# Optimization experiments

Measured on AMD Instinct MI355X. Metric: run time of the kernel, lower is better.

## Reference

```python
import jax, jax.numpy as jnp
import numpy as np

NEG_SLOPE = 0.2   # RGATConv default negative_slope
BN_EPS = 1e-5     # torch BatchNorm1d default eps


def _build_edges(n0, n1, batch):
    """Replicates generate_edges_union + PyG Batch offsetting. Returns [2, B*E] src/dst and [B*E] edge types."""
    n = n0 + n1
    def perm(k, off):  # itertools.permutations(range(k), 2) as (src, dst) columns
        a = np.repeat(np.arange(k), k); b = np.tile(np.arange(k), k)
        m = a != b
        return np.stack([a[m], b[m]]) + off
    intra = np.concatenate([perm(n0, 0), perm(n1, n0)], axis=1)                 # edge_type 0
    ca = np.repeat(np.arange(n0), n1); cb = np.tile(np.arange(n0, n), n0)
    cross = np.concatenate([np.stack([ca, cb]), np.stack([cb, ca])], axis=1)    # edge_type 1
    edges = np.concatenate([intra, cross], axis=1)
    etype = np.concatenate([np.zeros(intra.shape[1], np.int32), np.ones(cross.shape[1], np.int32)])
    offs = (np.arange(batch) * n)[:, None, None]
    edges_b = (edges[None, :, :] + offs).transpose(1, 0, 2).reshape(2, -1)      # per-graph node offsets
    etype_b = np.tile(etype, batch)
    return jnp.asarray(edges_b, jnp.int32), jnp.asarray(etype_b, jnp.int32)


def _segment_softmax(logits, seg, num_seg):
    m = jax.ops.segment_max(logits, seg, num_segments=num_seg)
    m = jnp.where(jnp.isfinite(m), m, 0.0)
    e = jnp.exp(logits - m[seg])
    s = jax.ops.segment_sum(e, seg, num_segments=num_seg)
    return e / (s[seg] + 1e-16)  # PyG softmax eps


def _rgat_layer(x, src, dst, etype, W, q, k, b, num_nodes):
    # PyG RGATConv: heads=1, dim=1, concat=False, additive-self-attention, across-relation softmax, aggr=add
    H = jnp.einsum('nf,rfe->rne', x, W)            # relation-specific transform: [2, BN, F]
    qs = jnp.einsum('rne,e->rn', H, q)             # q-score per node per relation
    ks = jnp.einsum('rne,e->rn', H, k)
    logit = jax.nn.leaky_relu(qs[etype, dst] + ks[etype, src], NEG_SLOPE)  # [E]
    alpha = _segment_softmax(logit, dst, num_nodes)
    msg = alpha[:, None] * H[etype, src]           # [E, F] per-edge messages
    out = jax.ops.segment_sum(msg, dst, num_segments=num_nodes)
    return out + b                                 # heads=1 -> mean over heads is identity; + bias


def setup_inputs() -> dict:
    key = jax.random.key(0)
    ks = jax.random.split(key, 6)
    B, F, N0, N1, L = 4, 256, 128, 128, 3
    s = 0.05
    return {
        'desc0': jax.random.normal(ks[0], (B, F, N0), jnp.float32),
        'desc1': jax.random.normal(ks[1], (B, F, N1), jnp.float32),
        'conv_w': jax.random.normal(ks[2], (L, 2, F, F), jnp.float32) * s,
        'conv_q': jax.random.normal(ks[3], (L, F), jnp.float32) * s,
        'conv_k': jax.random.normal(ks[4], (L, F), jnp.float32) * s,
        'conv_b': jnp.zeros((L, F), jnp.float32),
        'lin_w': jax.random.normal(ks[5], (L, F, 2 * F), jnp.float32) * s,
        'lin_b': jnp.zeros((L, F), jnp.float32),
        'bn_w': jnp.ones((L, F), jnp.float32),
        'bn_b': jnp.zeros((L, F), jnp.float32),
    }


def reference(desc0, desc1, conv_w, conv_q, conv_k, conv_b, lin_w, lin_b, bn_w, bn_b):
    b, f, n0 = desc0.shape
    n1 = desc1.shape[2]
    n = n0 + n1
    # [B, F, N] -> batched node features [B*N, F]
    x = jnp.concatenate([desc0, desc1], axis=2).transpose(0, 2, 1).reshape(b * n, f)
    edges, etype = _build_edges(n0, n1, b)
    src, dst = edges[0], edges[1]
    num_nodes = b * n
    for i in range(conv_w.shape[0]):
        msg1 = jax.nn.relu(_rgat_layer(x, src, dst, etype, conv_w[i], conv_q[i], conv_k[i], conv_b[i], num_nodes))
        msg2 = jnp.concatenate([x, msg1], axis=1) @ lin_w[i].T + lin_b[i]
        mu = msg2.mean(axis=0)
        var = msg2.var(axis=0)  # biased, as torch BatchNorm uses for normalization (training mode)
        msg3 = bn_w[i] * (msg2 - mu) / jnp.sqrt(var + BN_EPS) + bn_b[i]
        x = x + msg3            # edge_pool[i] == 1 -> no knn_graph rebuild
    x = x.reshape(b, n, f).transpose(0, 2, 1)
    return x[:, :, :n0], x[:, :, n0:]
```

## Files before the change

### kernel.cpp

```cpp
#include <hip/hip_runtime.h>
#include <math.h>


typedef __attribute__((ext_vector_type(8))) short short8;
typedef __attribute__((ext_vector_type(4))) float f32x4;
typedef unsigned short u16;
typedef unsigned int   u32;

__device__ __forceinline__ u16 f2bf(float f) {
    union { float f; u32 u; } v; v.f = f;
    u32 r = v.u + 0x7fffu + ((v.u >> 16) & 1u);
    return (u16)(r >> 16);
}
__device__ __forceinline__ short8 ld8(const u16* p) {
    return __builtin_bit_cast(short8, *(const int4*)p);
}

__global__ __launch_bounds__(256) void k_prep(
    const float* __restrict__ d0, const float* __restrict__ d1,
    const float* __restrict__ conv_w, const float* __restrict__ lin_w,
    float* __restrict__ x, u16* __restrict__ xb,
    u16* __restrict__ Wt, u16* __restrict__ lwb) {
    const int t = threadIdx.x;
    if (blockIdx.x < 256) {
        __shared__ float Ts[32 * 33];
        const int tt = blockIdx.x;
        const int b = tt >> 6, rem = tt & 63, ft = rem >> 3, nt = rem & 7;
        const float* src = (nt < 4) ? d0 : d1;
        const int nloc = (nt & 3) * 32;
        {
            int fr = t >> 3, c4 = t & 7;
            float4 v = *(const float4*)&src[b * 32768 + (ft * 32 + fr) * 128 + nloc + c4 * 4];
            Ts[fr * 33 + c4 * 4 + 0] = v.x;
            Ts[fr * 33 + c4 * 4 + 1] = v.y;
            Ts[fr * 33 + c4 * 4 + 2] = v.z;
            Ts[fr * 33 + c4 * 4 + 3] = v.w;
        }
        __syncthreads();
        {
            int nr = t >> 3, f4 = t & 7;
            float4 v;
            v.x = Ts[(f4 * 4 + 0) * 33 + nr];
            v.y = Ts[(f4 * 4 + 1) * 33 + nr];
            v.z = Ts[(f4 * 4 + 2) * 33 + nr];
            v.w = Ts[(f4 * 4 + 3) * 33 + nr];
            int node = b * 256 + nt * 32 + nr;
            int idx = node * 256 + ft * 32 + f4 * 4;
            *(float4*)&x[idx] = v;
            ushort4 hb = {f2bf(v.x), f2bf(v.y), f2bf(v.z), f2bf(v.w)};
            *(ushort4*)&xb[idx] = hb;
        }
    } else if (blockIdx.x < 640) {
        __shared__ float Ts[32 * 33];
        const int tt = blockIdx.x - 256;
        const int mat = tt >> 6, rem = tt & 63, et = rem >> 3, ft = rem & 7;
        {
            int fr = t >> 3, c4 = t & 7;
            float4 v = *(const float4*)&conv_w[mat * 65536 + (ft * 32 + fr) * 256 + et * 32 + c4 * 4];
            Ts[fr * 33 + c4 * 4 + 0] = v.x;
            Ts[fr * 33 + c4 * 4 + 1] = v.y;
            Ts[fr * 33 + c4 * 4 + 2] = v.z;
            Ts[fr * 33 + c4 * 4 + 3] = v.w;
        }
        __syncthreads();
        {
            int er = t >> 3, f4 = t & 7;
            ushort4 hb;
            hb.x = f2bf(Ts[(f4 * 4 + 0) * 33 + er]);
            hb.y = f2bf(Ts[(f4 * 4 + 1) * 33 + er]);
            hb.z = f2bf(Ts[(f4 * 4 + 2) * 33 + er]);
            hb.w = f2bf(Ts[(f4 * 4 + 3) * 33 + er]);
            *(ushort4*)&Wt[mat * 65536 + (et * 32 + er) * 256 + ft * 32 + f4 * 4] = hb;
        }
    } else {
        int o4 = (blockIdx.x - 640) * 256 + t;
        float4 v = *(const float4*)&lin_w[o4 * 4];
        ushort4 hb = {f2bf(v.x), f2bf(v.y), f2bf(v.z), f2bf(v.w)};
        *(ushort4*)&lwb[o4 * 4] = hb;
    }
}

__global__ __launch_bounds__(256, 1) void k_hqk(
    const float* __restrict__ xprev, const float* __restrict__ msg2,
    const float* __restrict__ sums, const float* __restrict__ sumsq,
    const float* __restrict__ bw, const float* __restrict__ bb,
    const u16* __restrict__ cwt,
    const float* __restrict__ cq, const float* __restrict__ ck,
    float* __restrict__ xcur, u16* __restrict__ xb, u16* __restrict__ Ht,
    float* __restrict__ qpart, float* __restrict__ kpart, int do_bn) {
    __shared__ __align__(16) u16 Asub[16 * 264];
    __shared__ __align__(16) float sc[256];
    __shared__ __align__(16) float sh[256];
    const int tid = threadIdx.x;
    const int mt = blockIdx.x >> 2, eg = blockIdx.x & 3;
    const int m0 = mt * 16;
    const int lane = tid & 63, widx = tid >> 6;
    const int row = lane & 15, kg = lane >> 4;

    if (do_bn) {
        float s1 = 0.f, s2 = 0.f;
        #pragma unroll 8
        for (int c = 0; c < 64; ++c) { s1 += sums[c * 256 + tid]; s2 += sumsq[c * 256 + tid]; }
        float mu  = s1 * (1.f / 1024.f);
        float var = s2 * (1.f / 1024.f) - mu * mu;
        float scale = bw[tid] * rsqrtf(var + 1e-5f);
        sc[tid] = scale;
        sh[tid] = bb[tid] - mu * scale;
    }
    __syncthreads();
    #pragma unroll
    for (int p = 0; p < 4; ++p) {
        const int r = p * 4 + (tid >> 6);
        const int c0 = (tid & 63) * 4;
        const int idx = (m0 + r) * 256 + c0;
        float4 v = *(const float4*)&xprev[idx];
        if (do_bn) {
            float4 m = *(const float4*)&msg2[idx];
            float4 s4 = *(const float4*)&sc[c0];
            float4 h4 = *(const float4*)&sh[c0];
            v.x += m.x * s4.x + h4.x;
            v.y += m.y * s4.y + h4.y;
            v.z += m.z * s4.z + h4.z;
            v.w += m.w * s4.w + h4.w;
        }
        ushort4 hb = {f2bf(v.x), f2bf(v.y), f2bf(v.z), f2bf(v.w)};
        *(ushort4*)&Asub[r * 264 + c0] = hb;
        if (do_bn && eg == 0) {
            *(float4*)&xcur[idx] = v;
            *(ushort4*)&xb[idx] = hb;
        }
    }
    __syncthreads();

    const int et = eg * 4 + widx, e0 = et * 16;
    const u16* B0 = cwt + (e0 + row) * 256 + kg * 8;
    const u16* B1 = B0 + 65536;
    const u16* Ap = &Asub[row * 264 + kg * 8];
    f32x4 acc0 = {0.f,0.f,0.f,0.f}, acc1 = {0.f,0.f,0.f,0.f};
    #pragma unroll
    for (int k0 = 0; k0 < 256; k0 += 32) {
        short8 a = ld8(Ap + k0);
        acc0 = __builtin_amdgcn_mfma_f32_16x16x32_bf16(a, ld8(B0 + k0), acc0, 0, 0, 0);
        acc1 = __builtin_amdgcn_mfma_f32_16x16x32_bf16(a, ld8(B1 + k0), acc1, 0, 0, 0);
    }
    ushort4 o0, o1;
    o0.x = f2bf(acc0[0]); o0.y = f2bf(acc0[1]); o0.z = f2bf(acc0[2]); o0.w = f2bf(acc0[3]);
    o1.x = f2bf(acc1[0]); o1.y = f2bf(acc1[1]); o1.z = f2bf(acc1[2]); o1.w = f2bf(acc1[3]);
    *(ushort4*)(Ht + (e0 + row) * 1024 + m0 + kg * 4) = o0;
    *(ushort4*)(Ht + 262144 + (e0 + row) * 1024 + m0 + kg * 4) = o1;
    float qe = cq[e0 + row], ke = ck[e0 + row];
    float pq0[4], pk0[4], pq1[4], pk1[4];
    #pragma unroll
    for (int c = 0; c < 4; ++c) {
        pq0[c] = acc0[c] * qe; pk0[c] = acc0[c] * ke;
        pq1[c] = acc1[c] * qe; pk1[c] = acc1[c] * ke;
    }
    #pragma unroll
    for (int off = 1; off < 16; off <<= 1) {
        #pragma unroll
        for (int c = 0; c < 4; ++c) {
            pq0[c] += __shfl_xor(pq0[c], off);
            pk0[c] += __shfl_xor(pk0[c], off);
            pq1[c] += __shfl_xor(pq1[c], off);
            pk1[c] += __shfl_xor(pk1[c], off);
        }
    }
    if (row == 0) {
        float4 a4 = {pq0[0], pq0[1], pq0[2], pq0[3]};
        float4 b4 = {pk0[0], pk0[1], pk0[2], pk0[3]};
        float4 c4 = {pq1[0], pq1[1], pq1[2], pq1[3]};
        float4 d4 = {pk1[0], pk1[1], pk1[2], pk1[3]};
        *(float4*)&qpart[et * 1024 + m0 + kg * 4] = a4;
        *(float4*)&kpart[et * 1024 + m0 + kg * 4] = b4;
        *(float4*)&qpart[(16 + et) * 1024 + m0 + kg * 4] = c4;
        *(float4*)&kpart[(16 + et) * 1024 + m0 + kg * 4] = d4;
    }
}

__global__ __launch_bounds__(256, 1) void k_attn(
    const float* __restrict__ qpart, const float* __restrict__ kpart,
    const u16* __restrict__ Ht, const float* __restrict__ cb,
    u16* __restrict__ msg1b) {
    __shared__ __align__(16) u16 Atile[16 * 264];
    __shared__ float ksl[2][256];
    __shared__ float qsl[2][16];
    __shared__ __align__(16) float T[4][16 * 20];
    const int tid = threadIdx.x;
    const int mt = blockIdx.x >> 2, eg = blockIdx.x & 3;
    const int m0 = mt * 16;
    const int g = mt >> 4, a = (mt >> 3) & 1;
    {
        float k0s = 0.f, k1s = 0.f;
        #pragma unroll
        for (int c = 0; c < 16; ++c) {
            k0s += kpart[c * 1024 + g * 256 + tid];
            k1s += kpart[(16 + c) * 1024 + g * 256 + tid];
        }
        ksl[0][tid] = k0s; ksl[1][tid] = k1s;
    }
    if (tid < 32) {
        int rel = tid >> 4, r = tid & 15;
        float q = 0.f;
        #pragma unroll
        for (int c = 0; c < 16; ++c) q += qpart[(rel * 16 + c) * 1024 + m0 + r];
        qsl[rel][r] = q;
    }
    __syncthreads();
    {
        const int r = tid >> 4, j = tid & 15;
        const int dl = (m0 + r) & 255;
        const int s0 = j * 16;
        const int rel = ((s0 >> 7) == a) ? 0 : 1;
        float qv = qsl[rel][r];
        float l[16], mx = -1e30f;
        #pragma unroll
        for (int i2 = 0; i2 < 16; ++i2) {
            float v = qv + ksl[rel][s0 + i2];
            v = (v >= 0.f) ? v : 0.2f * v;
            if (s0 + i2 == dl) v = -1e30f;
            l[i2] = v; mx = fmaxf(mx, v);
        }
        #pragma unroll
        for (int off = 1; off < 16; off <<= 1) mx = fmaxf(mx, __shfl_xor(mx, off));
        float s = 0.f;
        #pragma unroll
        for (int i2 = 0; i2 < 16; ++i2) { l[i2] = __expf(l[i2] - mx); s += l[i2]; }
        #pragma unroll
        for (int off = 1; off < 16; off <<= 1) s += __shfl_xor(s, off);
        float inv = 1.f / (s + 1e-16f);
        #pragma unroll
        for (int i2 = 0; i2 < 16; i2 += 2) {
            u32 p = (u32)f2bf(l[i2] * inv) | ((u32)f2bf(l[i2 + 1] * inv) << 16);
            *(u32*)&Atile[r * 264 + s0 + i2] = p;
        }
    }
    __syncthreads();
    const int lane = tid & 63, widx = tid >> 6;
    const int row = lane & 15, kg = lane >> 4;
    const int et = eg * 4 + widx, e0 = et * 16;
    const u16* Ap = &Atile[row * 264 + kg * 8];
    f32x4 acc = {0.f,0.f,0.f,0.f};
    #pragma unroll
    for (int k0 = 0; k0 < 256; k0 += 32) {
        const int rel = (((k0 >> 7) & 1) == a) ? 0 : 1;
        const u16* B = Ht + rel * 262144 + (e0 + row) * 1024 + g * 256 + k0 + kg * 8;
        acc = __builtin_amdgcn_mfma_f32_16x16x32_bf16(ld8(Ap + k0), ld8(B), acc, 0, 0, 0);
    }
    float bias = cb[e0 + row];
    float* Tw = &T[widx][0];
    #pragma unroll
    for (int c = 0; c < 4; ++c)
        Tw[(kg * 4 + c) * 20 + row] = fmaxf(acc[c] + bias, 0.f);
    __syncthreads();
    float4 v = *(float4*)&Tw[row * 20 + kg * 4];
    u32 lo = (u32)f2bf(v.x) | ((u32)f2bf(v.y) << 16);
    u32 hi = (u32)f2bf(v.z) | ((u32)f2bf(v.w) << 16);
    uint2 ov = {lo, hi};
    *(uint2*)(msg1b + (m0 + row) * 256 + e0 + kg * 4) = ov;
}

__global__ __launch_bounds__(256, 1) void k_lin(
    const u16* __restrict__ xb, const u16* __restrict__ msg1b,
    const u16* __restrict__ lwp, const float* __restrict__ lb,
    float* __restrict__ msg2, float* __restrict__ sums, float* __restrict__ sumsq) {
    __shared__ __align__(16) float T[4][16 * 20];
    const int tid = threadIdx.x, lane = tid & 63, widx = tid >> 6;
    const int row = lane & 15, kg = lane >> 4;
    const int mt = blockIdx.x >> 2, ng = blockIdx.x & 3;
    const int m0 = mt * 16;
    const int nt = ng * 4 + widx, n0 = nt * 16;
    const u16* A0 = xb    + (m0 + row) * 256 + kg * 8;
    const u16* A1 = msg1b + (m0 + row) * 256 + kg * 8;
    const u16* B  = lwp + (n0 + row) * 512 + kg * 8;
    f32x4 acc = {0.f,0.f,0.f,0.f};
    #pragma unroll
    for (int k0 = 0; k0 < 512; k0 += 32) {
        short8 av = (k0 < 256) ? ld8(A0 + k0) : ld8(A1 + (k0 - 256));
        acc = __builtin_amdgcn_mfma_f32_16x16x32_bf16(av, ld8(B + k0), acc, 0, 0, 0);
    }
    float bias = lb[n0 + row];
    float v0 = acc[0] + bias, v1 = acc[1] + bias, v2 = acc[2] + bias, v3 = acc[3] + bias;
    float s1 = v0 + v1 + v2 + v3;
    float s2 = v0 * v0 + v1 * v1 + v2 * v2 + v3 * v3;
    s1 += __shfl_xor(s1, 16); s1 += __shfl_xor(s1, 32);
    s2 += __shfl_xor(s2, 16); s2 += __shfl_xor(s2, 32);
    if (lane < 16) {
        sums [mt * 256 + n0 + lane] = s1;
        sumsq[mt * 256 + n0 + lane] = s2;
    }
    float* Tw = &T[widx][0];
    Tw[(kg * 4 + 0) * 20 + row] = v0;
    Tw[(kg * 4 + 1) * 20 + row] = v1;
    Tw[(kg * 4 + 2) * 20 + row] = v2;
    Tw[(kg * 4 + 3) * 20 + row] = v3;
    __syncthreads();
    float4 vv = *(float4*)&Tw[row * 20 + kg * 4];
    *(float4*)&msg2[(m0 + row) * 256 + n0 + kg * 4] = vv;
}

__global__ __launch_bounds__(256) void k_fin(
    const float* __restrict__ x2, const float* __restrict__ msg2,
    const float* __restrict__ sums, const float* __restrict__ sumsq,
    const float* __restrict__ bw, const float* __restrict__ bb,
    float* __restrict__ out) {
    __shared__ float Tt[32 * 33];
    __shared__ float ps1[32 * 9];
    __shared__ float ps2[32 * 9];
    __shared__ float scf[32];
    __shared__ float shf[32];
    const int t = threadIdx.x;
    const int nt2 = blockIdx.x >> 3, ft = blockIdx.x & 7;
    const int n0 = nt2 * 32, f0 = ft * 32;
    {
        const int fl = t & 31, chunk = t >> 5;
        float s1 = 0.f, s2 = 0.f;
        #pragma unroll
        for (int j = 0; j < 8; ++j) {
            s1 += sums [(chunk * 8 + j) * 256 + f0 + fl];
            s2 += sumsq[(chunk * 8 + j) * 256 + f0 + fl];
        }
        ps1[fl * 9 + chunk] = s1;
        ps2[fl * 9 + chunk] = s2;
    }
    __syncthreads();
    if (t < 32) {
        float s1 = 0.f, s2 = 0.f;
        #pragma unroll
        for (int c = 0; c < 8; ++c) { s1 += ps1[t * 9 + c]; s2 += ps2[t * 9 + c]; }
        float mu  = s1 * (1.f / 1024.f);
        float var = s2 * (1.f / 1024.f) - mu * mu;
        float scale = bw[f0 + t] * rsqrtf(var + 1e-5f);
        scf[t] = scale;
        shf[t] = bb[f0 + t] - mu * scale;
    }
    __syncthreads();
    {
        const int nr = t >> 3, f4 = t & 7;
        const int idx = (n0 + nr) * 256 + f0 + f4 * 4;
        float4 v = *(const float4*)&x2[idx];
        float4 m = *(const float4*)&msg2[idx];
        v.x += m.x * scf[f4 * 4 + 0] + shf[f4 * 4 + 0];
        v.y += m.y * scf[f4 * 4 + 1] + shf[f4 * 4 + 1];
        v.z += m.z * scf[f4 * 4 + 2] + shf[f4 * 4 + 2];
        v.w += m.w * scf[f4 * 4 + 3] + shf[f4 * 4 + 3];
        Tt[(f4 * 4 + 0) * 33 + nr] = v.x;
        Tt[(f4 * 4 + 1) * 33 + nr] = v.y;
        Tt[(f4 * 4 + 2) * 33 + nr] = v.z;
        Tt[(f4 * 4 + 3) * 33 + nr] = v.w;
    }
    __syncthreads();
    {
        const int fr = t >> 3, n4 = t & 7;
        const int b = n0 >> 8, half = (n0 >> 7) & 1, nloc = n0 & 127;
        float4 v;
        v.x = Tt[fr * 33 + n4 * 4 + 0];
        v.y = Tt[fr * 33 + n4 * 4 + 1];
        v.z = Tt[fr * 33 + n4 * 4 + 2];
        v.w = Tt[fr * 33 + n4 * 4 + 3];
        *(float4*)&out[half * 131072 + b * 32768 + (f0 + fr) * 128 + nloc + n4 * 4] = v;
    }
}

extern "C" void kernel_launch(void* const* d_in, const int* in_sizes, int n_in,
                              void* d_out, int out_size, void* d_ws, size_t ws_size,
                              hipStream_t stream) {
    const float* desc0  = (const float*)d_in[0];
    const float* desc1  = (const float*)d_in[1];
    const float* conv_w = (const float*)d_in[2];
    const float* conv_q = (const float*)d_in[3];
    const float* conv_k = (const float*)d_in[4];
    const float* conv_b = (const float*)d_in[5];
    const float* lin_w  = (const float*)d_in[6];
    const float* lin_b  = (const float*)d_in[7];
    const float* bn_w   = (const float*)d_in[8];
    const float* bn_b   = (const float*)d_in[9];
    float* out = (float*)d_out;

    char* p = (char*)d_ws;
    float* x0     = (float*)p; p += 1048576;
    float* x1     = (float*)p; p += 1048576;
    u16*   xb     = (u16*)p;   p += 524288;
    u16*   Wt     = (u16*)p;   p += 786432;
    u16*   lwb    = (u16*)p;   p += 786432;
    u16*   Ht     = (u16*)p;   p += 1048576;
    float* qpart  = (float*)p; p += 131072;
    float* kpart  = (float*)p; p += 131072;
    u16*   msg1b  = (u16*)p;   p += 524288;
    float* msg2   = (float*)p; p += 1048576;
    float* sums   = (float*)p; p += 65536;
    float* sumsq  = (float*)p; p += 65536;

    k_prep<<<1024, 256, 0, stream>>>(desc0, desc1, conv_w, lin_w, x0, xb, Wt, lwb);

    float* xs[4] = {x0, x0, x1, x0};
    for (int i = 0; i < 3; ++i) {
        const u16*   cwt = Wt + i * 131072;
        const u16*   lwp = lwb + i * 131072;
        const float* cq = conv_q + i * 256;
        const float* ck = conv_k + i * 256;
        const float* cb = conv_b + i * 256;
        const float* lb = lin_b + i * 256;
        const float* bwp = bn_w + (i ? (i - 1) * 256 : 0);
        const float* bbp = bn_b + (i ? (i - 1) * 256 : 0);

        k_hqk<<<256, 256, 0, stream>>>(xs[i], msg2, sums, sumsq, bwp, bbp,
                                       cwt, cq, ck, xs[i + 1], xb, Ht,
                                       qpart, kpart, i > 0 ? 1 : 0);
        k_attn<<<256, 256, 0, stream>>>(qpart, kpart, Ht, cb, msg1b);
        k_lin<<<256, 256, 0, stream>>>(xb, msg1b, lwp, lb, msg2, sums, sumsq);
    }

    k_fin<<<256, 256, 0, stream>>>(xs[3], msg2, sums, sumsq,
                                   bn_w + 512, bn_b + 512, out);
}
```

Before: 140.9 us.

## Split hqk/lin grids finer and accumulate BN stats with global atomics

k_hqk now gives each block a single relation, doubling the grid to 512 blocks, and k_lin runs 512 blocks of 128 threads. BatchNorm partial sums are no longer written per tile and re-reduced by every consumer block. They are accumulated into 256-entry global sums with atomicAdd, zeroed by k_attn block 0 before k_lin runs. This removes the 64-way partial reads in k_hqk and k_fin and adds parallelism, at the cost of atomic contention and float-sum order nondeterminism.

```diff
diff --git a/kernel.cpp b/kernel.cpp
--- a/kernel.cpp
+++ b/kernel.cpp
@@ -82,7 +82,7 @@
 
 __global__ __launch_bounds__(256, 1) void k_hqk(
     const float* __restrict__ xprev, const float* __restrict__ msg2,
-    const float* __restrict__ sums, const float* __restrict__ sumsq,
+    const float* __restrict__ gsum, const float* __restrict__ gsumsq,
     const float* __restrict__ bw, const float* __restrict__ bb,
     const u16* __restrict__ cwt,
     const float* __restrict__ cq, const float* __restrict__ ck,
@@ -92,15 +92,14 @@
     __shared__ __align__(16) float sc[256];
     __shared__ __align__(16) float sh[256];
     const int tid = threadIdx.x;
-    const int mt = blockIdx.x >> 2, eg = blockIdx.x & 3;
+    const int mt = blockIdx.x >> 3, sg = blockIdx.x & 7;
+    const int rel = sg >> 2, eg = sg & 3;
     const int m0 = mt * 16;
     const int lane = tid & 63, widx = tid >> 6;
     const int row = lane & 15, kg = lane >> 4;
 
     if (do_bn) {
-        float s1 = 0.f, s2 = 0.f;
-        #pragma unroll 8
-        for (int c = 0; c < 64; ++c) { s1 += sums[c * 256 + tid]; s2 += sumsq[c * 256 + tid]; }
+        float s1 = gsum[tid], s2 = gsumsq[tid];
         float mu  = s1 * (1.f / 1024.f);
         float var = s2 * (1.f / 1024.f) - mu * mu;
         float scale = bw[tid] * rsqrtf(var + 1e-5f);
@@ -125,7 +124,7 @@
         }
         ushort4 hb = {f2bf(v.x), f2bf(v.y), f2bf(v.z), f2bf(v.w)};
         *(ushort4*)&Asub[r * 264 + c0] = hb;
-        if (do_bn && eg == 0) {
+        if (do_bn && sg == 0) {
             *(float4*)&xcur[idx] = v;
             *(ushort4*)&xb[idx] = hb;
         }
@@ -133,54 +132,39 @@
     __syncthreads();
 
     const int et = eg * 4 + widx, e0 = et * 16;
-    const u16* B0 = cwt + (e0 + row) * 256 + kg * 8;
-    const u16* B1 = B0 + 65536;
+    const u16* B = cwt + rel * 65536 + (e0 + row) * 256 + kg * 8;
     const u16* Ap = &Asub[row * 264 + kg * 8];
-    f32x4 acc0 = {0.f,0.f,0.f,0.f}, acc1 = {0.f,0.f,0.f,0.f};
-    #pragma unroll
-    for (int k0 = 0; k0 < 256; k0 += 32) {
-        short8 a = ld8(Ap + k0);
-        acc0 = __builtin_amdgcn_mfma_f32_16x16x32_bf16(a, ld8(B0 + k0), acc0, 0, 0, 0);
-        acc1 = __builtin_amdgcn_mfma_f32_16x16x32_bf16(a, ld8(B1 + k0), acc1, 0, 0, 0);
-    }
-    ushort4 o0, o1;
-    o0.x = f2bf(acc0[0]); o0.y = f2bf(acc0[1]); o0.z = f2bf(acc0[2]); o0.w = f2bf(acc0[3]);
-    o1.x = f2bf(acc1[0]); o1.y = f2bf(acc1[1]); o1.z = f2bf(acc1[2]); o1.w = f2bf(acc1[3]);
-    *(ushort4*)(Ht + (e0 + row) * 1024 + m0 + kg * 4) = o0;
-    *(ushort4*)(Ht + 262144 + (e0 + row) * 1024 + m0 + kg * 4) = o1;
+    f32x4 acc = {0.f,0.f,0.f,0.f};
+    #pragma unroll
+    for (int k0 = 0; k0 < 256; k0 += 32)
+        acc = __builtin_amdgcn_mfma_f32_16x16x32_bf16(ld8(Ap + k0), ld8(B + k0), acc, 0, 0, 0);
+    ushort4 o0;
+    o0.x = f2bf(acc[0]); o0.y = f2bf(acc[1]); o0.z = f2bf(acc[2]); o0.w = f2bf(acc[3]);
+    *(ushort4*)(Ht + rel * 262144 + (e0 + row) * 1024 + m0 + kg * 4) = o0;
     float qe = cq[e0 + row], ke = ck[e0 + row];
-    float pq0[4], pk0[4], pq1[4], pk1[4];
-    #pragma unroll
-    for (int c = 0; c < 4; ++c) {
-        pq0[c] = acc0[c] * qe; pk0[c] = acc0[c] * ke;
-        pq1[c] = acc1[c] * qe; pk1[c] = acc1[c] * ke;
-    }
+    float pq[4], pk[4];
+    #pragma unroll
+    for (int c = 0; c < 4; ++c) { pq[c] = acc[c] * qe; pk[c] = acc[c] * ke; }
     #pragma unroll
     for (int off = 1; off < 16; off <<= 1) {
         #pragma unroll
         for (int c = 0; c < 4; ++c) {
-            pq0[c] += __shfl_xor(pq0[c], off);
-            pk0[c] += __shfl_xor(pk0[c], off);
-            pq1[c] += __shfl_xor(pq1[c], off);
-            pk1[c] += __shfl_xor(pk1[c], off);
+            pq[c] += __shfl_xor(pq[c], off);
+            pk[c] += __shfl_xor(pk[c], off);
         }
     }
     if (row == 0) {
-        float4 a4 = {pq0[0], pq0[1], pq0[2], pq0[3]};
-        float4 b4 = {pk0[0], pk0[1], pk0[2], pk0[3]};
-        float4 c4 = {pq1[0], pq1[1], pq1[2], pq1[3]};
-        float4 d4 = {pk1[0], pk1[1], pk1[2], pk1[3]};
-        *(float4*)&qpart[et * 1024 + m0 + kg * 4] = a4;
-        *(float4*)&kpart[et * 1024 + m0 + kg * 4] = b4;
-        *(float4*)&qpart[(16 + et) * 1024 + m0 + kg * 4] = c4;
-        *(float4*)&kpart[(16 + et) * 1024 + m0 + kg * 4] = d4;
+        float4 a4 = {pq[0], pq[1], pq[2], pq[3]};
+        float4 b4 = {pk[0], pk[1], pk[2], pk[3]};
+        *(float4*)&qpart[(rel * 16 + et) * 1024 + m0 + kg * 4] = a4;
+        *(float4*)&kpart[(rel * 16 + et) * 1024 + m0 + kg * 4] = b4;
     }
 }
 
 __global__ __launch_bounds__(256, 1) void k_attn(
     const float* __restrict__ qpart, const float* __restrict__ kpart,
     const u16* __restrict__ Ht, const float* __restrict__ cb,
-    u16* __restrict__ msg1b) {
+    u16* __restrict__ msg1b, float* __restrict__ gsum, float* __restrict__ gsumsq) {
     __shared__ __align__(16) u16 Atile[16 * 264];
     __shared__ float ksl[2][256];
     __shared__ float qsl[2][16];
@@ -189,6 +173,7 @@
     const int mt = blockIdx.x >> 2, eg = blockIdx.x & 3;
     const int m0 = mt * 16;
     const int g = mt >> 4, a = (mt >> 3) & 1;
+    if (blockIdx.x == 0) { gsum[tid] = 0.f; gsumsq[tid] = 0.f; }
     {
         float k0s = 0.f, k1s = 0.f;
         #pragma unroll
@@ -259,16 +244,16 @@
     *(uint2*)(msg1b + (m0 + row) * 256 + e0 + kg * 4) = ov;
 }
 
-__global__ __launch_bounds__(256, 1) void k_lin(
+__global__ __launch_bounds__(128, 1) void k_lin(
     const u16* __restrict__ xb, const u16* __restrict__ msg1b,
     const u16* __restrict__ lwp, const float* __restrict__ lb,
-    float* __restrict__ msg2, float* __restrict__ sums, float* __restrict__ sumsq) {
-    __shared__ __align__(16) float T[4][16 * 20];
+    float* __restrict__ msg2, float* __restrict__ gsum, float* __restrict__ gsumsq) {
+    __shared__ __align__(16) float T[2][16 * 20];
     const int tid = threadIdx.x, lane = tid & 63, widx = tid >> 6;
     const int row = lane & 15, kg = lane >> 4;
-    const int mt = blockIdx.x >> 2, ng = blockIdx.x & 3;
+    const int mt = blockIdx.x >> 3, ng = blockIdx.x & 7;
     const int m0 = mt * 16;
-    const int nt = ng * 4 + widx, n0 = nt * 16;
+    const int n0 = (ng * 2 + widx) * 16;
     const u16* A0 = xb    + (m0 + row) * 256 + kg * 8;
     const u16* A1 = msg1b + (m0 + row) * 256 + kg * 8;
     const u16* B  = lwp + (n0 + row) * 512 + kg * 8;
@@ -285,48 +270,31 @@
     s1 += __shfl_xor(s1, 16); s1 += __shfl_xor(s1, 32);
     s2 += __shfl_xor(s2, 16); s2 += __shfl_xor(s2, 32);
     if (lane < 16) {
-        sums [mt * 256 + n0 + lane] = s1;
-        sumsq[mt * 256 + n0 + lane] = s2;
+        atomicAdd(&gsum[n0 + lane], s1);
+        atomicAdd(&gsumsq[n0 + lane], s2);
     }
     float* Tw = &T[widx][0];
     Tw[(kg * 4 + 0) * 20 + row] = v0;
     Tw[(kg * 4 + 1) * 20 + row] = v1;
     Tw[(kg * 4 + 2) * 20 + row] = v2;
     Tw[(kg * 4 + 3) * 20 + row] = v3;
-    __syncthreads();
     float4 vv = *(float4*)&Tw[row * 20 + kg * 4];
     *(float4*)&msg2[(m0 + row) * 256 + n0 + kg * 4] = vv;
 }
 
 __global__ __launch_bounds__(256) void k_fin(
     const float* __restrict__ x2, const float* __restrict__ msg2,
-    const float* __restrict__ sums, const float* __restrict__ sumsq,
+    const float* __restrict__ gsum, const float* __restrict__ gsumsq,
     const float* __restrict__ bw, const float* __restrict__ bb,
     float* __restrict__ out) {
     __shared__ float Tt[32 * 33];
-    __shared__ float ps1[32 * 9];
-    __shared__ float ps2[32 * 9];
     __shared__ float scf[32];
     __shared__ float shf[32];
     const int t = threadIdx.x;
     const int nt2 = blockIdx.x >> 3, ft = blockIdx.x & 7;
     const int n0 = nt2 * 32, f0 = ft * 32;
-    {
-        const int fl = t & 31, chunk = t >> 5;
-        float s1 = 0.f, s2 = 0.f;
-        #pragma unroll
-        for (int j = 0; j < 8; ++j) {
-            s1 += sums [(chunk * 8 + j) * 256 + f0 + fl];
-            s2 += sumsq[(chunk * 8 + j) * 256 + f0 + fl];
-        }
-        ps1[fl * 9 + chunk] = s1;
-        ps2[fl * 9 + chunk] = s2;
-    }
-    __syncthreads();
     if (t < 32) {
-        float s1 = 0.f, s2 = 0.f;
-        #pragma unroll
-        for (int c = 0; c < 8; ++c) { s1 += ps1[t * 9 + c]; s2 += ps2[t * 9 + c]; }
+        float s1 = gsum[f0 + t], s2 = gsumsq[f0 + t];
         float mu  = s1 * (1.f / 1024.f);
         float var = s2 * (1.f / 1024.f) - mu * mu;
         float scale = bw[f0 + t] * rsqrtf(var + 1e-5f);
@@ -387,8 +355,8 @@
     float* kpart  = (float*)p; p += 131072;
     u16*   msg1b  = (u16*)p;   p += 524288;
     float* msg2   = (float*)p; p += 1048576;
-    float* sums   = (float*)p; p += 65536;
-    float* sumsq  = (float*)p; p += 65536;
+    float* gsum   = (float*)p; p += 1024;
+    float* gsumsq = (float*)p; p += 1024;
 
     k_prep<<<1024, 256, 0, stream>>>(desc0, desc1, conv_w, lin_w, x0, xb, Wt, lwb);
 
@@ -403,13 +371,13 @@
         const float* bwp = bn_w + (i ? (i - 1) * 256 : 0);
         const float* bbp = bn_b + (i ? (i - 1) * 256 : 0);
 
-        k_hqk<<<256, 256, 0, stream>>>(xs[i], msg2, sums, sumsq, bwp, bbp,
+        k_hqk<<<512, 256, 0, stream>>>(xs[i], msg2, gsum, gsumsq, bwp, bbp,
                                        cwt, cq, ck, xs[i + 1], xb, Ht,
                                        qpart, kpart, i > 0 ? 1 : 0);
-        k_attn<<<256, 256, 0, stream>>>(qpart, kpart, Ht, cb, msg1b);
-        k_lin<<<256, 256, 0, stream>>>(xb, msg1b, lwp, lb, msg2, sums, sumsq);
-    }
-
-    k_fin<<<256, 256, 0, stream>>>(xs[3], msg2, sums, sumsq,
+        k_attn<<<256, 256, 0, stream>>>(qpart, kpart, Ht, cb, msg1b, gsum, gsumsq);
+        k_lin<<<512, 128, 0, stream>>>(xb, msg1b, lwp, lb, msg2, gsum, gsumsq);
+    }
+
+    k_fin<<<256, 256, 0, stream>>>(xs[3], msg2, gsum, gsumsq,
                                    bn_w + 512, bn_b + 512, out);
 }
```

After: 139.5 us. Within noise of the previous version (-1.0%).
